# Optimization experiments

Hardware: AMD Instinct MI355X
Metric: run time of the kernel (lower is better)

The kernel has to match this reference:

```python
import jax, jax.numpy as jnp
import numpy as np

B, C, H, W = 4, 256, 64, 64
CH = C // 2  # inner channels


def setup_inputs() -> dict:
    key = jax.random.key(0)
    ks = jax.random.split(key, 9)
    s_in = 1.0 / np.sqrt(C)
    s_w = 1.0 / np.sqrt(CH)
    return {
        "x": jax.random.normal(ks[0], (B, C, H, W), dtype=jnp.float32),
        "theta_w": jax.random.normal(ks[1], (CH, C), dtype=jnp.float32) * s_in,
        "theta_b": jax.random.normal(ks[2], (CH,), dtype=jnp.float32) * s_in,
        "phi_w": jax.random.normal(ks[3], (CH, C), dtype=jnp.float32) * s_in,
        "phi_b": jax.random.normal(ks[4], (CH,), dtype=jnp.float32) * s_in,
        "g_w": jax.random.normal(ks[5], (CH, C), dtype=jnp.float32) * s_in,
        "g_b": jax.random.normal(ks[6], (CH,), dtype=jnp.float32) * s_in,
        "W_w": jax.random.normal(ks[7], (C, CH), dtype=jnp.float32) * s_w,
        "W_b": jax.random.normal(ks[8], (C,), dtype=jnp.float32) * s_w,
    }


def _proj(x_flat, w, b):
    # 1x1 conv == channel matmul; x_flat: [B, C, N] -> [B, O, N]
    return jnp.einsum("oc,bcn->bon", w, x_flat) + b[None, :, None]


def reference(x, theta_w, theta_b, phi_w, phi_b, g_w, g_b, W_w, W_b):
    b, c, h, w = x.shape
    n = h * w
    xf = x.reshape(b, c, n)
    theta = _proj(xf, theta_w, theta_b)  # [B, CH, N]
    phi = _proj(xf, phi_w, phi_b)        # [B, CH, N]
    g = _proj(xf, g_w, g_b)              # [B, CH, N]
    # scores[b,i,j] = theta[:, :, i] . phi[:, :, j]; softmax over j
    attn = jax.nn.softmax(jnp.einsum("bci,bcj->bij", theta, phi), axis=-1)
    # torch: bmm(g_x, attn) -> out[b,c,i] = sum_j g[b,c,j] * attn[b,j,i]
    out = jnp.einsum("bcj,bji->bci", g, attn)  # [B, CH, N]
    out = jnp.einsum("oc,bcn->bon", W_w, out) + W_b[None, :, None]
    return out.reshape(b, c, h, w) + x
```

## Files before the change

kernel.cpp:

```cpp
#include <hip/hip_runtime.h>
#include <hip/hip_bf16.h>
#include <math.h>

#define BB    4
#define CC    256
#define CHN   128
#define NN    4096

typedef short short8 __attribute__((ext_vector_type(8)));
typedef float f32x4  __attribute__((ext_vector_type(4)));
typedef float f32x16 __attribute__((ext_vector_type(16)));
typedef unsigned short u16;
typedef u16  us4 __attribute__((ext_vector_type(4)));

#define MFMA16(a, b, c) __builtin_amdgcn_mfma_f32_16x16x32_bf16((a), (b), (c), 0, 0, 0)
#define MFMA32(a, b, c) __builtin_amdgcn_mfma_f32_32x32x16_bf16((a), (b), (c), 0, 0, 0)
#define LOG2E 1.4426950408889634f

#if __has_builtin(__builtin_amdgcn_exp2f)
#define EXP2F(x) __builtin_amdgcn_exp2f(x)
#else
#define EXP2F(x) exp2f(x)
#endif
#if __has_builtin(__builtin_amdgcn_rcpf)
#define RCPF(x) __builtin_amdgcn_rcpf(x)
#else
#define RCPF(x) (1.0f / (x))
#endif

static __device__ __forceinline__ u16 f2bf(float f) {
    union { float f; unsigned u; } v; v.f = f;
    unsigned r = v.u + 0x7FFFu + ((v.u >> 16) & 1u);
    return (u16)(r >> 16);
}
static __device__ __forceinline__ float bf2f(u16 h) {
    union { unsigned u; float f; } v; v.u = ((unsigned)h) << 16;
    return v.f;
}
static __device__ __forceinline__ unsigned pkbf(float a, float b) {
    __hip_bfloat162 h = __float22bfloat162_rn(make_float2(a, b));
    return *reinterpret_cast<unsigned*>(&h);
}
static __device__ __forceinline__ int sw128(int row, int u) {
    return row * 128 + ((u ^ (row & 15)) << 3);
}
static __device__ __forceinline__ void gload16(const u16* g, u16* l) {
    __builtin_amdgcn_global_load_lds(
        (const __attribute__((address_space(1))) void*)g,
        (__attribute__((address_space(3))) void*)l, 16, 0, 0);
}

typedef union { unsigned u[4]; short8 v; } bfrag;

#if __has_builtin(__builtin_amdgcn_permlane32_swap)
#define REPACK(sv, f) do { \
    unsigned e0 = pkbf(EXP2F(sv[0]),  EXP2F(sv[1])); \
    unsigned e1 = pkbf(EXP2F(sv[2]),  EXP2F(sv[3])); \
    unsigned e2 = pkbf(EXP2F(sv[4]),  EXP2F(sv[5])); \
    unsigned e3 = pkbf(EXP2F(sv[6]),  EXP2F(sv[7])); \
    unsigned e4 = pkbf(EXP2F(sv[8]),  EXP2F(sv[9])); \
    unsigned e5 = pkbf(EXP2F(sv[10]), EXP2F(sv[11])); \
    unsigned e6 = pkbf(EXP2F(sv[12]), EXP2F(sv[13])); \
    unsigned e7 = pkbf(EXP2F(sv[14]), EXP2F(sv[15])); \
    auto r02 = __builtin_amdgcn_permlane32_swap(e0, e2, false, false); \
    auto r13 = __builtin_amdgcn_permlane32_swap(e1, e3, false, false); \
    auto r46 = __builtin_amdgcn_permlane32_swap(e4, e6, false, false); \
    auto r57 = __builtin_amdgcn_permlane32_swap(e5, e7, false, false); \
    f[0].u[0] = r02[0]; f[0].u[1] = r13[0]; \
    f[0].u[2] = r02[1]; f[0].u[3] = r13[1]; \
    f[1].u[0] = r46[0]; f[1].u[1] = r57[0]; \
    f[1].u[2] = r46[1]; f[1].u[3] = r57[1]; \
} while (0)
#else
#define REPACK(sv, f) do { \
    unsigned e0 = pkbf(EXP2F(sv[0]),  EXP2F(sv[1])); \
    unsigned e1 = pkbf(EXP2F(sv[2]),  EXP2F(sv[3])); \
    unsigned e2 = pkbf(EXP2F(sv[4]),  EXP2F(sv[5])); \
    unsigned e3 = pkbf(EXP2F(sv[6]),  EXP2F(sv[7])); \
    unsigned e4 = pkbf(EXP2F(sv[8]),  EXP2F(sv[9])); \
    unsigned e5 = pkbf(EXP2F(sv[10]), EXP2F(sv[11])); \
    unsigned e6 = pkbf(EXP2F(sv[12]), EXP2F(sv[13])); \
    unsigned e7 = pkbf(EXP2F(sv[14]), EXP2F(sv[15])); \
    unsigned q0 = __shfl_xor(e0, 32), q1 = __shfl_xor(e1, 32); \
    unsigned q2 = __shfl_xor(e2, 32), q3 = __shfl_xor(e3, 32); \
    unsigned q4 = __shfl_xor(e4, 32), q5 = __shfl_xor(e5, 32); \
    unsigned q6 = __shfl_xor(e6, 32), q7 = __shfl_xor(e7, 32); \
    f[0].u[0] = lh ? q2 : e0;  f[0].u[1] = lh ? q3 : e1; \
    f[0].u[2] = lh ? e2 : q0;  f[0].u[3] = lh ? e3 : q1; \
    f[1].u[0] = lh ? q6 : e4;  f[1].u[1] = lh ? q7 : e5; \
    f[1].u[2] = lh ? e6 : q4;  f[1].u[3] = lh ? e7 : q5; \
} while (0)
#endif

__global__ __launch_bounds__(256) void k_cvtw(
    const float* __restrict__ tw, const float* __restrict__ pw,
    const float* __restrict__ gw, const float* __restrict__ Ww,
    u16* __restrict__ wall)
{
    int idx = (blockIdx.x * 256 + threadIdx.x) * 4;
    const float* s = (idx < 32768) ? tw
                   : (idx < 65536) ? pw
                   : (idx < 98304) ? gw : Ww;
    float sc = (idx < 32768) ? LOG2E : 1.0f;
    float4 v = *(const float4*)(s + (idx & 32767));
    us4 r = { f2bf(v.x * sc), f2bf(v.y * sc), f2bf(v.z * sc), f2bf(v.w * sc) };
    *(us4*)(wall + idx) = r;
}

__global__ __launch_bounds__(512) void k_proj(
    const float* __restrict__ x, const u16* __restrict__ wall,
    const float* __restrict__ tb, const float* __restrict__ pb,
    const float* __restrict__ gbias,
    u16* __restrict__ tht, u16* __restrict__ pht, u16* __restrict__ gg)
{
    __shared__ u16 xs[64 * 264];
    __shared__ u16 gbuf[128 * 68];
    const int tid = threadIdx.x;
    const int n0  = blockIdx.x * 64;
    const int b   = blockIdx.y;
    const int ln  = tid & 15, q = (tid >> 4) & 3, wid = tid >> 6;
    const int ow  = wid & 1, nw = wid >> 1;

    for (int p = 0; p < 8; ++p) {
        int id = p * 512 + tid;
        int c = id >> 4, n4 = (id & 15) * 4;
        float4 xv = *(const float4*)(x + ((size_t)b * CC + c) * NN + n0 + n4);
        xs[(n4 + 0) * 264 + c] = f2bf(xv.x);
        xs[(n4 + 1) * 264 + c] = f2bf(xv.y);
        xs[(n4 + 2) * 264 + c] = f2bf(xv.z);
        xs[(n4 + 3) * 264 + c] = f2bf(xv.w);
    }
    __syncthreads();

    short8 bfr[8];
    #pragma unroll
    for (int ks = 0; ks < 8; ++ks)
        bfr[ks] = *(const short8*)(&xs[(nw * 16 + ln) * 264 + ks * 32 + q * 8]);

    for (int pr = 0; pr < 3; ++pr) {
        const u16* wsrc = wall + pr * 32768;
        f32x4 acc[4];
        #pragma unroll
        for (int oo = 0; oo < 4; ++oo) acc[oo] = (f32x4){0.f, 0.f, 0.f, 0.f};
        for (int ks = 0; ks < 8; ++ks) {
            short8 a[4];
            #pragma unroll
            for (int oo = 0; oo < 4; ++oo)
                a[oo] = *(const short8*)(wsrc + (size_t)(ow*64 + oo*16 + ln) * 256 + ks*32 + q*8);
            #pragma unroll
            for (int oo = 0; oo < 4; ++oo)
                acc[oo] = MFMA16(a[oo], bfr[ks], acc[oo]);
        }
        const float* bias = (pr == 0) ? tb : (pr == 1 ? pb : gbias);
        const float bsc = (pr == 0) ? LOG2E : 1.0f;
        if (pr < 2) {
            u16* dst = (pr == 0) ? tht : pht;
            const int n = n0 + nw * 16 + ln;
            #pragma unroll
            for (int oo = 0; oo < 4; ++oo) {
                int o = ow * 64 + oo * 16 + q * 4;
                float4 bv = *(const float4*)(bias + o);
                f32x4 v = acc[oo];
                uint2 r = { pkbf(v.x + bv.x * bsc, v.y + bv.y * bsc),
                            pkbf(v.z + bv.z * bsc, v.w + bv.w * bsc) };
                *(uint2*)(dst + ((size_t)b * NN + n) * CHN + o) = r;
            }
        } else {
            const int nl = nw * 16 + ln;
            #pragma unroll
            for (int oo = 0; oo < 4; ++oo) {
                int o = ow * 64 + oo * 16 + q * 4;
                float4 bv = *(const float4*)(bias + o);
                f32x4 v = acc[oo];
                gbuf[(o + 0) * 68 + nl] = f2bf(v.x + bv.x);
                gbuf[(o + 1) * 68 + nl] = f2bf(v.y + bv.y);
                gbuf[(o + 2) * 68 + nl] = f2bf(v.z + bv.z);
                gbuf[(o + 3) * 68 + nl] = f2bf(v.w + bv.w);
            }
            __syncthreads();
            for (int p = 0; p < 4; ++p) {
                int id = p * 512 + tid;
                int c = id >> 4, n4 = (id & 15) * 4;
                us4 r = *(const us4*)(&gbuf[c * 68 + n4]);
                *(us4*)(gg + ((size_t)b * CHN + c) * NN + n0 + n4) = r;
            }
        }
    }
}

__global__ __launch_bounds__(512, 2) void k_rowsum(
    const u16* __restrict__ tht, const u16* __restrict__ pht,
    float* __restrict__ Z)
{
    __shared__ u16 ph_s[2][128 * 128];
    const int tid = threadIdx.x;
    const int j0  = blockIdx.x * 256;
    const int i00 = blockIdx.y * 1024;
    const int b   = blockIdx.z;
    const int l   = tid & 63, w = tid >> 6;
    const int lm  = l & 31, lh = l >> 5;
    const u16* thb = tht + (size_t)b * NN * CHN;
    const u16* phb = pht + (size_t)b * NN * CHN;

    short8 ar[8];
    #pragma unroll
    for (int ks = 0; ks < 8; ++ks)
        ar[ks] = *(const short8*)(thb + (size_t)(j0 + w*32 + lm) * CHN + ks*16 + lh*8);

    for (int p = 0; p < 4; ++p) {
        int id = p * 512 + tid;
        int row = id >> 4, u = id & 15;
        short8 v = *(const short8*)(phb + (size_t)(i00 + row) * CHN + u * 8);
        *(short8*)(&ph_s[0][sw128(row, u)]) = v;
    }

    float zp[16];
    #pragma unroll
    for (int r = 0; r < 16; ++r) zp[r] = 0.f;

    for (int is = 0; is < 8; ++is) {
        __syncthreads();
        if (is < 7) {
            for (int p = 0; p < 4; ++p) {
                int id = p * 512 + tid;
                int row = id >> 4, u = id & 15;
                short8 v = *(const short8*)(phb + (size_t)(i00 + (is+1)*128 + row) * CHN + u * 8);
                *(short8*)(&ph_s[(is + 1) & 1][sw128(row, u)]) = v;
            }
        }
        const u16* cur = ph_s[is & 1];

        #pragma unroll
        for (int ii = 0; ii < 4; ++ii) {
            f32x16 s;
            #pragma unroll
            for (int r = 0; r < 16; ++r) s[r] = 0.f;
            #pragma unroll
            for (int ks = 0; ks < 8; ++ks) {
                short8 bfrag = *(const short8*)(&cur[sw128(ii*32 + lm, ks*2 + lh)]);
                s = MFMA32(ar[ks], bfrag, s);
            }
            #pragma unroll
            for (int r = 0; r < 16; ++r) zp[r] += EXP2F(s[r]);
        }
    }

    float zr[16];
    #pragma unroll
    for (int r = 0; r < 16; ++r) {
        float v = zp[r];
        v += __shfl_xor(v, 1);
        v += __shfl_xor(v, 2);
        v += __shfl_xor(v, 4);
        v += __shfl_xor(v, 8);
        v += __shfl_xor(v, 16);
        zr[r] = v;
    }
    if (lm == 0) {
        #pragma unroll
        for (int r = 0; r < 16; ++r) {
            int j = j0 + w*32 + (r & 3) + 8*(r >> 2) + 4*lh;
            atomicAdd(&Z[(size_t)b * NN + j], zr[r]);
        }
    }
}

__global__ __launch_bounds__(256) void k_gdiv(
    const float* __restrict__ Z, u16* __restrict__ gg)
{
    int q = blockIdx.x * 256 + threadIdx.x;
    int b   = q >> 17;
    int rem = q & 131071;
    int c   = rem >> 10;
    int n4  = (rem & 1023) * 4;
    size_t base = ((size_t)b * CHN + c) * NN + n4;
    us4 g = *(const us4*)(gg + base);
    float4 z = *(const float4*)(Z + (size_t)b * NN + n4);
    us4 r = { f2bf(bf2f(g.x) * RCPF(z.x)), f2bf(bf2f(g.y) * RCPF(z.y)),
              f2bf(bf2f(g.z) * RCPF(z.z)), f2bf(bf2f(g.w) * RCPF(z.w)) };
    *(us4*)(gg + base) = r;
}

__global__ __launch_bounds__(512, 2) void k_attn(
    const u16* __restrict__ tht, const u16* __restrict__ pht,
    const u16* __restrict__ gg, u16* __restrict__ innerT)
{
    __shared__ u16 th_s[2][128 * 128];
    __shared__ u16 g_s [2][128 * 128];
    const int tid = threadIdx.x;
    const int i0  = blockIdx.x * 256;
    const int jq  = blockIdx.y;
    const int b   = blockIdx.z;
    const int w   = tid >> 6;
    const int lm  = tid & 31, lh = (tid >> 5) & 1;

    const u16*  thb = tht + (size_t)b * NN * CHN;
    const u16*  ggb = gg  + (size_t)b * CHN * NN;

    int offT[4], offG[4];
    #pragma unroll
    for (int p = 0; p < 4; ++p) {
        int row = p * 32 + (tid >> 4);
        int u   = (tid & 15) ^ (row & 15);
        offT[p] = row * CHN + u * 8;
        offG[p] = row * NN  + u * 8;
    }

    short8 phr[8];
    #pragma unroll
    for (int ks = 0; ks < 8; ++ks)
        phr[ks] = *(const short8*)(pht + ((size_t)b * NN + i0 + w*32 + lm) * CHN + ks*16 + lh*8);

    #pragma unroll
    for (int p = 0; p < 4; ++p) {
        gload16(thb + (size_t)(jq * 1024) * CHN + offT[p], &th_s[0][0] + p*4096 + (w << 9));
        gload16(ggb + jq * 1024 + offG[p],                 &g_s [0][0] + p*4096 + (w << 9));
    }
    __syncthreads();

    f32x16 pacc[4];
    #pragma unroll
    for (int ct = 0; ct < 4; ++ct)
        #pragma unroll
        for (int r = 0; r < 16; ++r) pacc[ct][r] = 0.f;

    for (int s = 0; s < 8; ++s) {
        const int j0s = jq * 1024 + s * 128;
        const u16* thc = th_s[s & 1];
        const u16* gc  = g_s [s & 1];

        if (s < 7) {
            const int nb = (s + 1) & 1;
            #pragma unroll
            for (int p = 0; p < 4; ++p) {
                gload16(thb + (size_t)(j0s + 128) * CHN + offT[p], &th_s[nb][0] + p*4096 + (w << 9));
                gload16(ggb + (j0s + 128) + offG[p],               &g_s [nb][0] + p*4096 + (w << 9));
            }
        }

        #pragma unroll
        for (int jj = 0; jj < 4; ++jj) {
            f32x16 sv;
            #pragma unroll
            for (int r = 0; r < 16; ++r) sv[r] = 0.f;
            #pragma unroll
            for (int ks = 0; ks < 8; ++ks) {
                short8 a = *(const short8*)(&thc[sw128(jj*32 + lm, ks*2 + lh)]);
                sv = MFMA32(a, phr[ks], sv);
            }
            bfrag f[2];
            REPACK(sv, f);
            #pragma unroll
            for (int h = 0; h < 2; ++h) {
                #pragma unroll
                for (int ct = 0; ct < 4; ++ct) {
                    short8 ag = *(const short8*)(&gc[sw128(ct*32 + lm, jj*4 + h*2 + lh)]);
                    pacc[ct] = MFMA32(ag, f[h].v, pacc[ct]);
                }
            }
        }
        __syncthreads();
    }

    u16* dst = innerT + ((size_t)jq * BB + b) * (size_t)NN * CHN;
    const int i = i0 + w*32 + lm;
    #pragma unroll
    for (int ct = 0; ct < 4; ++ct) {
        #pragma unroll
        for (int rq = 0; rq < 4; ++rq) {
            const int c0 = ct*32 + rq*8 + lh*4;
            uint2 r = { pkbf(pacc[ct][rq*4+0], pacc[ct][rq*4+1]),
                        pkbf(pacc[ct][rq*4+2], pacc[ct][rq*4+3]) };
            *(uint2*)(dst + (size_t)i * CHN + c0) = r;
        }
    }
}

__global__ __launch_bounds__(512, 2) void k_final(
    const u16* __restrict__ innerT, const float* __restrict__ x,
    const u16* __restrict__ Wwbf, const float* __restrict__ Wb,
    float* __restrict__ out)
{
    __shared__ u16 w_s[256 * 128];
    __shared__ u16 a_s[64 * 128];
    const int tid = threadIdx.x;
    const int n0  = blockIdx.x * 64;
    const int b   = blockIdx.y;
    const int l   = tid & 63, w = tid >> 6;
    const int lm  = l & 31, lh = l >> 5;

    for (int p = 0; p < 8; ++p) {
        int id = p * 512 + tid;
        int row = id >> 4, u = id & 15;
        *(short8*)(&w_s[sw128(row, u)]) = *(const short8*)(Wwbf + (size_t)row * CHN + u * 8);
    }
    __syncthreads();

    short8 aw[8];
    #pragma unroll
    for (int ks = 0; ks < 8; ++ks)
        aw[ks] = *(const short8*)(&w_s[sw128(w*32 + lm, ks*2 + lh)]);

    f32x16 acc[2];
    #pragma unroll
    for (int nt = 0; nt < 2; ++nt)
        #pragma unroll
        for (int r = 0; r < 16; ++r) acc[nt][r] = 0.f;

    for (int jq = 0; jq < 4; ++jq) {
        __syncthreads();
        for (int p = 0; p < 2; ++p) {
            int id = p * 512 + tid;
            int row = id >> 4, u = id & 15;
            *(short8*)(&a_s[sw128(row, u)]) =
                *(const short8*)(innerT + (((size_t)jq * BB + b) * NN + n0 + row) * CHN + u * 8);
        }
        __syncthreads();
        #pragma unroll
        for (int ks = 0; ks < 8; ++ks) {
            short8 bn[2];
            #pragma unroll
            for (int nt = 0; nt < 2; ++nt)
                bn[nt] = *(const short8*)(&a_s[sw128(nt*32 + lm, ks*2 + lh)]);
            acc[0] = MFMA32(aw[ks], bn[0], acc[0]);
            acc[1] = MFMA32(aw[ks], bn[1], acc[1]);
        }
    }

    #pragma unroll
    for (int nt = 0; nt < 2; ++nt) {
        const int n = n0 + nt*32 + lm;
        #pragma unroll
        for (int r = 0; r < 16; ++r) {
            const int o = w*32 + (r & 3) + 8*(r >> 2) + 4*lh;
            const size_t idx = ((size_t)b * CC + o) * NN + n;
            out[idx] = acc[nt][r] + Wb[o] + x[idx];
        }
    }
}

extern "C" void kernel_launch(void* const* d_in, const int* in_sizes, int n_in,
                              void* d_out, int out_size, void* d_ws, size_t ws_size,
                              hipStream_t stream)
{
    const float* x  = (const float*)d_in[0];
    const float* tw = (const float*)d_in[1];
    const float* tb = (const float*)d_in[2];
    const float* pw = (const float*)d_in[3];
    const float* pb = (const float*)d_in[4];
    const float* gw = (const float*)d_in[5];
    const float* gb = (const float*)d_in[6];
    const float* Ww = (const float*)d_in[7];
    const float* Wb = (const float*)d_in[8];
    float* out = (float*)d_out;

    char* p = (char*)d_ws;
    const size_t proj_u16 = (size_t)BB * NN * CHN;
    u16*   tht    = (u16*)p;   p += proj_u16 * 2;
    u16*   pht    = (u16*)p;   p += proj_u16 * 2;
    u16*   gg     = (u16*)p;   p += proj_u16 * 2;
    u16*   wall   = (u16*)p;   p += (size_t)131072 * 2;
    float* Z      = (float*)p; p += (size_t)BB * NN * 4;
    u16*   innerT = (u16*)p;

    hipMemsetAsync(Z, 0, (size_t)BB * NN * sizeof(float), stream);
    k_cvtw  <<<128, 256, 0, stream>>>(tw, pw, gw, Ww, wall);
    k_proj  <<<dim3(64, BB), 512, 0, stream>>>(x, wall, tb, pb, gb, tht, pht, gg);
    k_rowsum<<<dim3(16, 4, BB), 512, 0, stream>>>(tht, pht, Z);
    k_gdiv  <<<2048, 256, 0, stream>>>(Z, gg);
    k_attn  <<<dim3(16, 4, BB), 512, 0, stream>>>(tht, pht, gg, innerT);
    k_final <<<dim3(64, BB), 512, 0, stream>>>(innerT, x, wall + 98304, Wb, out);
}
```

Baseline: 188.1 us.

## Use async LDS loads with partial vmcnt waits in rowsum and attention kernels

Measured after the change: 191.1 us. About the same (+1.6%).

```diff
diff --git a/kernel.cpp b/kernel.cpp
--- a/kernel.cpp
+++ b/kernel.cpp
@@ -92,6 +92,10 @@
 } while (0)
 #endif
 
+#define WAITCNT_VM(n) asm volatile("s_waitcnt vmcnt(" #n ")" ::: "memory")
+#define RAW_BARRIER() do { __builtin_amdgcn_s_barrier(); \
+                           __builtin_amdgcn_sched_barrier(0); } while (0)
+
 __global__ __launch_bounds__(256) void k_cvtw(
     const float* __restrict__ tw, const float* __restrict__ pw,
     const float* __restrict__ gw, const float* __restrict__ Ww,
@@ -202,34 +206,43 @@
     const u16* thb = tht + (size_t)b * NN * CHN;
     const u16* phb = pht + (size_t)b * NN * CHN;
 
+    int offP[4];
+    #pragma unroll
+    for (int p = 0; p < 4; ++p) {
+        int row = p * 32 + (tid >> 4);
+        int u   = (tid & 15) ^ (row & 15);
+        offP[p] = row * CHN + u * 8;
+    }
+
     short8 ar[8];
     #pragma unroll
     for (int ks = 0; ks < 8; ++ks)
         ar[ks] = *(const short8*)(thb + (size_t)(j0 + w*32 + lm) * CHN + ks*16 + lh*8);
 
-    for (int p = 0; p < 4; ++p) {
-        int id = p * 512 + tid;
-        int row = id >> 4, u = id & 15;
-        short8 v = *(const short8*)(phb + (size_t)(i00 + row) * CHN + u * 8);
-        *(short8*)(&ph_s[0][sw128(row, u)]) = v;
-    }
+    #pragma unroll
+    for (int p = 0; p < 4; ++p)
+        gload16(phb + (size_t)i00 * CHN + offP[p], &ph_s[0][0] + p*4096 + (w << 9));
+    WAITCNT_VM(0);
+    RAW_BARRIER();
 
     float zp[16];
     #pragma unroll
     for (int r = 0; r < 16; ++r) zp[r] = 0.f;
 
     for (int is = 0; is < 8; ++is) {
-        __syncthreads();
         if (is < 7) {
-            for (int p = 0; p < 4; ++p) {
-                int id = p * 512 + tid;
-                int row = id >> 4, u = id & 15;
-                short8 v = *(const short8*)(phb + (size_t)(i00 + (is+1)*128 + row) * CHN + u * 8);
-                *(short8*)(&ph_s[(is + 1) & 1][sw128(row, u)]) = v;
-            }
-        }
+            const int nb = (is + 1) & 1;
+            #pragma unroll
+            for (int p = 0; p < 4; ++p)
+                gload16(phb + (size_t)(i00 + (is+1)*128) * CHN + offP[p],
+                        &ph_s[nb][0] + p*4096 + (w << 9));
+            WAITCNT_VM(4);
+        } else {
+            WAITCNT_VM(0);
+        }
+        RAW_BARRIER();
+
         const u16* cur = ph_s[is & 1];
-
         #pragma unroll
         for (int ii = 0; ii < 4; ++ii) {
             f32x16 s;
@@ -243,6 +256,7 @@
             #pragma unroll
             for (int r = 0; r < 16; ++r) zp[r] += EXP2F(s[r]);
         }
+        RAW_BARRIER();
     }
 
     float zr[16];
@@ -316,7 +330,8 @@
         gload16(thb + (size_t)(jq * 1024) * CHN + offT[p], &th_s[0][0] + p*4096 + (w << 9));
         gload16(ggb + jq * 1024 + offG[p],                 &g_s [0][0] + p*4096 + (w << 9));
     }
-    __syncthreads();
+    WAITCNT_VM(0);
+    RAW_BARRIER();
 
     f32x16 pacc[4];
     #pragma unroll
@@ -326,8 +341,6 @@
 
     for (int s = 0; s < 8; ++s) {
         const int j0s = jq * 1024 + s * 128;
-        const u16* thc = th_s[s & 1];
-        const u16* gc  = g_s [s & 1];
 
         if (s < 7) {
             const int nb = (s + 1) & 1;
@@ -336,8 +349,14 @@
                 gload16(thb + (size_t)(j0s + 128) * CHN + offT[p], &th_s[nb][0] + p*4096 + (w << 9));
                 gload16(ggb + (j0s + 128) + offG[p],               &g_s [nb][0] + p*4096 + (w << 9));
             }
-        }
-
+            WAITCNT_VM(8);
+        } else {
+            WAITCNT_VM(0);
+        }
+        RAW_BARRIER();
+
+        const u16* thc = th_s[s & 1];
+        const u16* gc  = g_s [s & 1];
         #pragma unroll
         for (int jj = 0; jj < 4; ++jj) {
             f32x16 sv;
@@ -359,7 +378,7 @@
                 }
             }
         }
-        __syncthreads();
+        RAW_BARRIER();
     }
 
     u16* dst = innerT + ((size_t)jq * BB + b) * (size_t)NN * CHN;
```
